# Optimization experiments

Measured on AMD Instinct MI355X. Metric: run time of the kernel, lower is better.

The kernel has to match this reference:

```python
import jax, jax.numpy as jnp
import numpy as np

B, S, HIDDEN = 2, 2048, 1024
HEADS, HEAD_DIM = 16, 64
GRID_SIZE, SPLINE_ORDER = 5, 3  # efficient-kan defaults


def b_splines(x, grid, k=SPLINE_ORDER):
    """x: (N, in), grid: (in, GRID_SIZE + 2k + 1) -> (N, in, GRID_SIZE + k)."""
    xe = x[..., None]
    bases = ((xe >= grid[:, :-1]) & (xe < grid[:, 1:])).astype(x.dtype)
    for p in range(1, k + 1):  # Cox-de Boor recursion, fixed small loop
        left = (xe - grid[:, : -(p + 1)]) / (grid[:, p:-1] - grid[:, : -(p + 1)]) * bases[..., :-1]
        right = (grid[:, p + 1:] - xe) / (grid[:, p + 1:] - grid[:, 1:-p]) * bases[..., 1:]
        bases = left + right
    return bases


def setup_inputs() -> dict:
    key = jax.random.key(0)
    ks = jax.random.split(key, 7)
    h = 2.0 / GRID_SIZE  # grid_range = [-1, 1]
    grid_1d = (jnp.arange(-SPLINE_ORDER, GRID_SIZE + SPLINE_ORDER + 1, dtype=jnp.float32) * h - 1.0)
    grid = jnp.tile(grid_1d[None, :], (HIDDEN, 1))  # (in, 12)
    return {
        "x": jax.random.normal(ks[0], (B, S, HIDDEN), jnp.float32),
        "base_weight": jax.random.normal(ks[1], (3 * HIDDEN, HIDDEN), jnp.float32) * 0.02,
        "spline_weight": jax.random.normal(ks[2], (3 * HIDDEN, HIDDEN, GRID_SIZE + SPLINE_ORDER), jnp.float32) * 0.02,
        "spline_scaler": jax.random.normal(ks[3], (3 * HIDDEN, HIDDEN), jnp.float32) * 0.1 + 1.0,
        "grid": grid,
        "rotation_matrix": jax.random.normal(ks[4], (HEAD_DIM, HEAD_DIM), jnp.float32) / np.sqrt(HEAD_DIM),
        "out_w": jax.random.normal(ks[5], (HIDDEN, HIDDEN), jnp.float32) * 0.02,
        "out_b": jnp.zeros((HIDDEN,), jnp.float32),
    }


def reference(x, base_weight, spline_weight, spline_scaler, grid, rotation_matrix, out_w, out_b):
    Bc, Sc, Hc = x.shape
    xf = x.reshape(-1, Hc)  # (N, in)
    # KANLinear: silu base branch + B-spline branch
    base = jax.nn.silu(xf) @ base_weight.T  # (N, 3H)
    bs = b_splines(xf, grid)  # (N, in, G+k)
    sw = spline_weight * spline_scaler[..., None]  # scaled spline weight
    spline = bs.reshape(bs.shape[0], -1) @ sw.reshape(sw.shape[0], -1).T
    qkv = (base + spline).reshape(Bc, Sc, HEADS, 3 * HEAD_DIM).transpose(0, 2, 1, 3)
    q, k, v = jnp.split(qkv, 3, axis=-1)  # each (B,H,S,dh)
    # RoPE via full learned rotation matrix
    qr = jnp.einsum('bhsd,md->bhsm', q, rotation_matrix)
    kr = jnp.einsum('bhsd,md->bhsm', k, rotation_matrix)
    scores = jnp.einsum('bhsm,bhtm->bhst', qr, kr) / (HEAD_DIM ** 0.5)
    attn = jax.nn.softmax(scores, axis=-1)
    ctx = jnp.einsum('bhst,bhtd->bhsd', attn, v)
    ctx = ctx.transpose(0, 2, 1, 3).reshape(Bc, Sc, Hc)
    return ctx @ out_w.T + out_b
```

## Files before the change

### kernel.cpp

```cpp
#include <hip/hip_runtime.h>
#include <cstdint>
#include <cstddef>

typedef __bf16 bf16;
typedef bf16  bf16x8 __attribute__((ext_vector_type(8)));
typedef float f32x4  __attribute__((ext_vector_type(4)));

#define GLOBAL_AS __attribute__((address_space(1)))
#define LDS_AS    __attribute__((address_space(3)))

__device__ __forceinline__ void ldg_lds16(const void* g, void* l) {
  __builtin_amdgcn_global_load_lds((const GLOBAL_AS void*)g, (LDS_AS void*)l, 16, 0, 0);
}

constexpr int NB    = 2;
constexpr int SQ    = 2048;
constexpr int HID   = 1024;
constexpr int NHEAD = 16;
constexpr int HD    = 64;
constexpr int NROW  = NB * SQ;
constexpr int KA    = HID + HID * 8;
constexpr int NO    = 3 * HID;

__global__ __launch_bounds__(256) void build_a(const float* __restrict__ X,
                                               const float* __restrict__ Grid,
                                               bf16* __restrict__ A) {
  int idx = blockIdx.x * 256 + threadIdx.x;
  int n = idx >> 10, i = idx & 1023;
  float x = X[idx];
  float s = x / (1.0f + __expf(-x));
  A[(size_t)n * KA + i] = (bf16)s;

  float kn[12];
#pragma unroll
  for (int t = 0; t < 12; t++) kn[t] = Grid[i * 12 + t];
  float bs[11];
#pragma unroll
  for (int t = 0; t < 11; t++) bs[t] = (x >= kn[t] && x < kn[t + 1]) ? 1.0f : 0.0f;
#pragma unroll
  for (int p = 1; p <= 3; p++) {
#pragma unroll
    for (int t = 0; t + p < 11; t++) {
      bs[t] = (x - kn[t]) / (kn[t + p] - kn[t]) * bs[t]
            + (kn[t + p + 1] - x) / (kn[t + p + 1] - kn[t + 1]) * bs[t + 1];
    }
  }
  union { bf16 h[8]; uint4 u; } pk;
#pragma unroll
  for (int t = 0; t < 8; t++) pk.h[t] = (bf16)bs[t];
  *(uint4*)(A + (size_t)n * KA + HID + i * 8) = pk.u;
}

__global__ __launch_bounds__(256) void build_w(const float* __restrict__ BW,
                                               const float* __restrict__ SW,
                                               const float* __restrict__ SS,
                                               bf16* __restrict__ Wp) {
  int idx = blockIdx.x * 256 + threadIdx.x;
  int o = idx / 1152;
  int jc = idx - o * 1152;
  float4 f0, f1;
  if (jc < 128) {
    f0 = *(const float4*)(BW + (size_t)o * HID + jc * 8);
    f1 = *(const float4*)(BW + (size_t)o * HID + jc * 8 + 4);
  } else {
    int ii = jc - 128;
    float sc = SS[(size_t)o * HID + ii];
    f0 = *(const float4*)(SW + ((size_t)o * HID + ii) * 8);
    f1 = *(const float4*)(SW + ((size_t)o * HID + ii) * 8 + 4);
    f0.x *= sc; f0.y *= sc; f0.z *= sc; f0.w *= sc;
    f1.x *= sc; f1.y *= sc; f1.z *= sc; f1.w *= sc;
  }
  union { bf16 h[8]; uint4 u; } pk;
  pk.h[0] = (bf16)f0.x; pk.h[1] = (bf16)f0.y; pk.h[2] = (bf16)f0.z; pk.h[3] = (bf16)f0.w;
  pk.h[4] = (bf16)f1.x; pk.h[5] = (bf16)f1.y; pk.h[6] = (bf16)f1.z; pk.h[7] = (bf16)f1.w;
  *(uint4*)(Wp + (size_t)o * KA + jc * 8) = pk.u;
}

__global__ __launch_bounds__(256) void conv_wout(const float* __restrict__ OW,
                                                 bf16* __restrict__ WOB) {
  int i = (blockIdx.x * 256 + threadIdx.x) * 4;
  float4 f = *(const float4*)(OW + i);
  union { bf16 h[4]; uint2 u; } p;
  p.h[0] = (bf16)f.x; p.h[1] = (bf16)f.y; p.h[2] = (bf16)f.z; p.h[3] = (bf16)f.w;
  *(uint2*)(WOB + i) = p.u;
}

__global__ __launch_bounds__(256) void compute_m(const float* __restrict__ R,
                                                 bf16* __restrict__ Mb) {
  __shared__ float Rl[64 * 64];
  int tid = threadIdx.x;
  for (int idx = tid; idx < 4096; idx += 256) Rl[idx] = R[idx];
  __syncthreads();
  int d = tid >> 2;
  int e0 = (tid & 3) * 16;
#pragma unroll
  for (int j = 0; j < 16; j++) {
    int e = e0 + j;
    float acc = 0.f;
#pragma unroll
    for (int m = 0; m < 64; m++) acc += Rl[m * 64 + d] * Rl[m * 64 + e];
    Mb[d * 64 + e] = (bf16)(0.125f * acc);
  }
}

template <int K>
__device__ __forceinline__ void gemm_tile(const bf16* __restrict__ A,
                                          const bf16* __restrict__ Bw,
                                          int rowBase, int colBase,
                                          bf16* As, bf16* Bs, f32x4 acc[4][4]) {
  const int tid  = threadIdx.x;
  const int lane = tid & 63, wave = tid >> 6;
  const int wm = (wave >> 1) * 64, wn = (wave & 1) * 64;
  const int l15 = lane & 15, quad = lane >> 4;
  const int rA = tid >> 2;
  const int swSrc = ((tid & 3) ^ ((rA >> 1) & 3)) * 8;
  const int swRd  = (quad ^ ((l15 >> 1) & 3)) * 8;
#pragma unroll
  for (int mi = 0; mi < 4; mi++)
#pragma unroll
    for (int ni = 0; ni < 4; ni++) acc[mi][ni] = (f32x4){0.f, 0.f, 0.f, 0.f};

  const bf16* Ag1 = A  + (size_t)(rowBase + rA) * K + swSrc;
  const bf16* Ag2 = A  + (size_t)(rowBase + 64 + rA) * K + swSrc;
  const bf16* Bg1 = Bw + (size_t)(colBase + rA) * K + swSrc;
  const bf16* Bg2 = Bw + (size_t)(colBase + 64 + rA) * K + swSrc;

  for (int k0 = 0; k0 < K; k0 += 32) {
    __syncthreads();
    ldg_lds16(Ag1 + k0, As + tid * 8);
    ldg_lds16(Ag2 + k0, As + 2048 + tid * 8);
    ldg_lds16(Bg1 + k0, Bs + tid * 8);
    ldg_lds16(Bg2 + k0, Bs + 2048 + tid * 8);
    __syncthreads();
    bf16x8 af[4], bfr[4];
#pragma unroll
    for (int mi = 0; mi < 4; mi++)
      af[mi] = *(const bf16x8*)(As + (wm + mi * 16 + l15) * 32 + swRd);
#pragma unroll
    for (int ni = 0; ni < 4; ni++)
      bfr[ni] = *(const bf16x8*)(Bs + (wn + ni * 16 + l15) * 32 + swRd);
#pragma unroll
    for (int mi = 0; mi < 4; mi++)
#pragma unroll
      for (int ni = 0; ni < 4; ni++)
        acc[mi][ni] = __builtin_amdgcn_mfma_f32_16x16x32_bf16(af[mi], bfr[ni], acc[mi][ni], 0, 0, 0);
  }
}

__global__ __launch_bounds__(256) void gemm_qkv(const bf16* __restrict__ A,
                                                const bf16* __restrict__ W,
                                                bf16* __restrict__ QQ,
                                                bf16* __restrict__ KK,
                                                bf16* __restrict__ VV) {
  __shared__ __align__(16) bf16 As[128 * 32];
  __shared__ __align__(16) bf16 Bs[128 * 32];
  f32x4 acc[4][4];
  const int rowBase = blockIdx.y * 128, colBase = blockIdx.x * 128;
  gemm_tile<KA>(A, W, rowBase, colBase, As, Bs, acc);

  const int tid = threadIdx.x, lane = tid & 63, wave = tid >> 6;
  const int wm = (wave >> 1) * 64, wn = (wave & 1) * 64;
  const int l15 = lane & 15, quad = lane >> 4;
#pragma unroll
  for (int mi = 0; mi < 4; mi++)
#pragma unroll
    for (int ni = 0; ni < 4; ni++)
#pragma unroll
      for (int r = 0; r < 4; r++) {
        int row = rowBase + wm + mi * 16 + quad * 4 + r;
        int col = colBase + wn + ni * 16 + l15;
        int b = row >> 11, s = row & 2047;
        int hh = col / 192, c = col - hh * 192;
        size_t base = ((size_t)(b * NHEAD + hh) * SQ + s) * HD;
        float v = acc[mi][ni][r];
        if (c < 64)        QQ[base + c] = (bf16)v;
        else if (c < 128)  KK[base + c - 64] = (bf16)v;
        else               VV[base + c - 128] = (bf16)v;
      }
}

__global__ __launch_bounds__(256) void transpose_v(const bf16* __restrict__ VV,
                                                   bf16* __restrict__ VT) {
  __shared__ __align__(16) bf16 Ts[64 * 72];
  const int st = blockIdx.x, bh = blockIdx.y, tid = threadIdx.x;
  const bf16* src = VV + ((size_t)bh * SQ + st * 64) * HD;
#pragma unroll
  for (int i = 0; i < 2; i++) {
    int c = i * 256 + tid, row = c >> 3, seg = c & 7;
    bf16x8 v8 = *(const bf16x8*)(src + row * HD + seg * 8);
    *(bf16x8*)(&Ts[row * 72 + seg * 8]) = v8;
  }
  __syncthreads();
#pragma unroll
  for (int i = 0; i < 2; i++) {
    int c = i * 256 + tid, drow = c >> 3, seg = c & 7;
    bf16x8 o8;
#pragma unroll
    for (int j = 0; j < 8; j++) o8[j] = Ts[(seg * 8 + j) * 72 + drow];
    *(bf16x8*)(VT + ((size_t)bh * HD + drow) * SQ + st * 64 + seg * 8) = o8;
  }
}

__global__ __launch_bounds__(256) void attn(const bf16* __restrict__ QQ,
                                            const bf16* __restrict__ KK,
                                            const bf16* __restrict__ VT,
                                            const bf16* __restrict__ Mb,
                                            bf16* __restrict__ CTXB) {
  __shared__ __align__(16) bf16 Qs[128 * 64];
  __shared__ __align__(16) bf16 Ks[128 * 64];
  __shared__ __align__(16) bf16 Vt[64 * 128];
  __shared__ __align__(16) bf16 Ps[128 * 64];
  __shared__ __align__(16) bf16 Ms[64 * 64];
  const int bh = blockIdx.y;
  const int b = bh >> 4, h = bh & 15;
  const int qbase = blockIdx.x * 128;
  const bf16* Q  = QQ + (size_t)bh * SQ * HD;
  const bf16* Kp = KK + (size_t)bh * SQ * HD;
  const bf16* Vp = VT + (size_t)bh * HD * SQ;
  const int tid = threadIdx.x, lane = tid & 63, wave = tid >> 6;
  const int l15 = lane & 15, quad = lane >> 4;
  const int sw8 = l15 & 7;
  const float SHIFT = 12.0f;

#pragma unroll
  for (int i = 0; i < 4; i++) {
    int c = i * 256 + tid, row = c >> 3, seg = c & 7;
    ldg_lds16(Q + (size_t)(qbase + row) * HD + ((seg ^ (row & 7)) * 8), Qs + c * 8);
  }
#pragma unroll
  for (int i = 0; i < 2; i++) {
    int c = i * 256 + tid, row = c >> 3, seg = c & 7;
    ldg_lds16(Mb + row * 64 + ((seg ^ (row & 7)) * 8), Ms + c * 8);
  }
  __syncthreads();

  {
    f32x4 racc[2][4];
#pragma unroll
    for (int mi = 0; mi < 2; mi++)
#pragma unroll
      for (int nj = 0; nj < 4; nj++) racc[mi][nj] = (f32x4){0.f, 0.f, 0.f, 0.f};
#pragma unroll
    for (int kc = 0; kc < 2; kc++) {
      const int slot = ((kc * 4 + quad) ^ sw8) * 8;
      bf16x8 aq[2], bm[4];
#pragma unroll
      for (int mi = 0; mi < 2; mi++)
        aq[mi] = *(const bf16x8*)(Qs + (wave * 32 + mi * 16 + l15) * 64 + slot);
#pragma unroll
      for (int nj = 0; nj < 4; nj++)
        bm[nj] = *(const bf16x8*)(Ms + (nj * 16 + l15) * 64 + slot);
#pragma unroll
      for (int mi = 0; mi < 2; mi++)
#pragma unroll
        for (int nj = 0; nj < 4; nj++)
          racc[mi][nj] = __builtin_amdgcn_mfma_f32_16x16x32_bf16(aq[mi], bm[nj], racc[mi][nj], 0, 0, 0);
    }
#pragma unroll
    for (int mi = 0; mi < 2; mi++)
#pragma unroll
      for (int nj = 0; nj < 4; nj++)
#pragma unroll
        for (int r = 0; r < 4; r++) {
          int qrow = wave * 32 + mi * 16 + quad * 4 + r;
          int slot = ((nj * 2 + (l15 >> 3)) ^ (qrow & 7)) * 8 + (l15 & 7);
          Qs[qrow * 64 + slot] = (bf16)racc[mi][nj][r];
        }
  }
  bf16x8 qf[2][2];
#pragma unroll
  for (int kc = 0; kc < 2; kc++)
#pragma unroll
    for (int mi = 0; mi < 2; mi++)
      qf[mi][kc] = *(const bf16x8*)(Qs + (wave * 32 + mi * 16 + l15) * 64 + (((kc * 4 + quad) ^ sw8) * 8));

  float lpart[2][4];
  f32x4 ctxacc[2][4];
#pragma unroll
  for (int mi = 0; mi < 2; mi++)
#pragma unroll
    for (int r = 0; r < 4; r++) lpart[mi][r] = 0.f;
#pragma unroll
  for (int mi = 0; mi < 2; mi++)
#pragma unroll
    for (int nd = 0; nd < 4; nd++) ctxacc[mi][nd] = (f32x4){0.f, 0.f, 0.f, 0.f};

  for (int kt = 0; kt < SQ / 128; kt++) {
    const int kbase = kt * 128;
    if (kt) __syncthreads();
#pragma unroll
    for (int i = 0; i < 4; i++) {
      int c = i * 256 + tid, row = c >> 3, seg = c & 7;
      ldg_lds16(Kp + (size_t)(kbase + row) * HD + ((seg ^ (row & 7)) * 8), Ks + c * 8);
    }
#pragma unroll
    for (int i = 0; i < 4; i++) {
      int c = i * 256 + tid, row = c >> 4, seg = c & 15;
      ldg_lds16(Vp + (size_t)row * SQ + kbase + ((seg ^ (row & 7)) * 8), Vt + c * 8);
    }
    __syncthreads();

#pragma unroll
    for (int hh = 0; hh < 2; hh++) {
      f32x4 sacc[2][4];
#pragma unroll
      for (int mi = 0; mi < 2; mi++)
#pragma unroll
        for (int nj = 0; nj < 4; nj++) sacc[mi][nj] = (f32x4){0.f, 0.f, 0.f, 0.f};
#pragma unroll
      for (int kc = 0; kc < 2; kc++) {
        const int slot = ((kc * 4 + quad) ^ sw8) * 8;
        bf16x8 bfr[4];
#pragma unroll
        for (int nj = 0; nj < 4; nj++)
          bfr[nj] = *(const bf16x8*)(Ks + (hh * 64 + nj * 16 + l15) * 64 + slot);
#pragma unroll
        for (int mi = 0; mi < 2; mi++)
#pragma unroll
          for (int nj = 0; nj < 4; nj++)
            sacc[mi][nj] = __builtin_amdgcn_mfma_f32_16x16x32_bf16(qf[mi][kc], bfr[nj], sacc[mi][nj], 0, 0, 0);
      }
#pragma unroll
      for (int mi = 0; mi < 2; mi++)
#pragma unroll
        for (int nj = 0; nj < 4; nj++)
#pragma unroll
          for (int r = 0; r < 4; r++) {
            float p = __expf(sacc[mi][nj][r] - SHIFT);
            lpart[mi][r] += p;
            int prow = wave * 32 + mi * 16 + quad * 4 + r;
            int slot = ((nj * 2 + (l15 >> 3)) ^ (prow & 7)) * 8 + (l15 & 7);
            Ps[prow * 64 + slot] = (bf16)p;
          }
#pragma unroll
      for (int kc = 0; kc < 2; kc++) {
        const int aslot = ((kc * 4 + quad) ^ sw8) * 8;
        const int vslot = (((hh * 8 + kc * 4 + quad)) ^ sw8) * 8;
        bf16x8 af[2], bfr[4];
#pragma unroll
        for (int mi = 0; mi < 2; mi++)
          af[mi] = *(const bf16x8*)(Ps + (wave * 32 + mi * 16 + l15) * 64 + aslot);
#pragma unroll
        for (int nd = 0; nd < 4; nd++)
          bfr[nd] = *(const bf16x8*)(Vt + (nd * 16 + l15) * 128 + vslot);
#pragma unroll
        for (int mi = 0; mi < 2; mi++)
#pragma unroll
          for (int nd = 0; nd < 4; nd++)
            ctxacc[mi][nd] = __builtin_amdgcn_mfma_f32_16x16x32_bf16(af[mi], bfr[nd], ctxacc[mi][nd], 0, 0, 0);
      }
    }
  }

#pragma unroll
  for (int mi = 0; mi < 2; mi++)
#pragma unroll
    for (int r = 0; r < 4; r++) {
      float l = lpart[mi][r];
#pragma unroll
      for (int off = 1; off < 16; off <<= 1) l += __shfl_xor(l, off);
      float inv = 1.0f / l;
#pragma unroll
      for (int nd = 0; nd < 4; nd++) {
        int srow = qbase + wave * 32 + mi * 16 + quad * 4 + r;
        float val = ctxacc[mi][nd][r] * inv;
        CTXB[(size_t)(b * SQ + srow) * HID + h * HD + nd * 16 + l15] = (bf16)val;
      }
    }
}

__global__ __launch_bounds__(256) void gemm_out(const bf16* __restrict__ CTX,
                                                const bf16* __restrict__ WOB,
                                                const float* __restrict__ OB,
                                                float* __restrict__ OUT) {
  __shared__ __align__(16) bf16 As[128 * 32];
  __shared__ __align__(16) bf16 Bs[128 * 32];
  f32x4 acc[4][4];
  const int rowBase = blockIdx.y * 128, colBase = blockIdx.x * 128;
  gemm_tile<HID>(CTX, WOB, rowBase, colBase, As, Bs, acc);

  const int tid = threadIdx.x, lane = tid & 63, wave = tid >> 6;
  const int wm = (wave >> 1) * 64, wn = (wave & 1) * 64;
  const int l15 = lane & 15, quad = lane >> 4;
#pragma unroll
  for (int mi = 0; mi < 4; mi++)
#pragma unroll
    for (int ni = 0; ni < 4; ni++)
#pragma unroll
      for (int r = 0; r < 4; r++) {
        int row = rowBase + wm + mi * 16 + quad * 4 + r;
        int col = colBase + wn + ni * 16 + l15;
        OUT[(size_t)row * HID + col] = acc[mi][ni][r] + OB[col];
      }
}

extern "C" void kernel_launch(void* const* d_in, const int* in_sizes, int n_in,
                              void* d_out, int out_size, void* d_ws, size_t ws_size,
                              hipStream_t stream) {
  const float* x    = (const float*)d_in[0];
  const float* bw   = (const float*)d_in[1];
  const float* sw   = (const float*)d_in[2];
  const float* ss   = (const float*)d_in[3];
  const float* grid = (const float*)d_in[4];
  const float* rot  = (const float*)d_in[5];
  const float* ow   = (const float*)d_in[6];
  const float* ob   = (const float*)d_in[7];
  float* out = (float*)d_out;

  char* ws = (char*)d_ws;
  bf16* Aact = (bf16*)(ws);
  bf16* vt   = (bf16*)(ws);
  bf16* Mb   = (bf16*)(ws + 8388608);
  bf16* Wp   = (bf16*)(ws + 75497472);
  bf16* qq   = (bf16*)(ws + 132120576);
  bf16* kk   = (bf16*)(ws + 140509184);
  bf16* vv   = (bf16*)(ws + 148897792);
  bf16* ctxb = (bf16*)(ws + 157286400);
  bf16* wob  = (bf16*)(ws + 165675008);

  build_a<<<NROW * HID / 256, 256, 0, stream>>>(x, grid, Aact);
  build_w<<<NO * (KA / 8) / 256, 256, 0, stream>>>(bw, sw, ss, Wp);
  conv_wout<<<HID * HID / 1024, 256, 0, stream>>>(ow, wob);
  gemm_qkv<<<dim3(NO / 128, NROW / 128), 256, 0, stream>>>(Aact, Wp, qq, kk, vv);
  compute_m<<<1, 256, 0, stream>>>(rot, Mb);
  transpose_v<<<dim3(SQ / 64, NB * NHEAD), 256, 0, stream>>>(vv, vt);
  attn<<<dim3(SQ / 128, NB * NHEAD), 256, 0, stream>>>(qq, kk, vt, Mb, ctxb);
  gemm_out<<<dim3(HID / 128, NROW / 128), 256, 0, stream>>>(ctxb, wob, ob, out);
}
```

Before: 631.2 us.

## Rewrite QKV GEMM with 256x192 tiles, double-buffered BK=64 LDS pipeline

Replaces the 128x128, BK=32 single-buffered QKV GEMM with a 512-thread kernel using 256x192 tiles (one head per column block), BK=64, XOR-swizzled LDS, and double-buffered async global-to-LDS loads overlapped with MFMA. Aligning the column tile to one head simplifies the scatter epilogue, and the larger tile raises operand reuse. The cost is heavier register and LDS use (about 112KB LDS per block) and a smaller grid of 256 blocks, which may hurt occupancy and load balance.

```diff
diff --git a/kernel.cpp b/kernel.cpp
--- a/kernel.cpp
+++ b/kernel.cpp
@@ -147,32 +147,116 @@
   }
 }
 
-__global__ __launch_bounds__(256) void gemm_qkv(const bf16* __restrict__ A,
-                                                const bf16* __restrict__ W,
-                                                bf16* __restrict__ QQ,
-                                                bf16* __restrict__ KK,
-                                                bf16* __restrict__ VV) {
-  __shared__ __align__(16) bf16 As[128 * 32];
-  __shared__ __align__(16) bf16 Bs[128 * 32];
-  f32x4 acc[4][4];
-  const int rowBase = blockIdx.y * 128, colBase = blockIdx.x * 128;
-  gemm_tile<KA>(A, W, rowBase, colBase, As, Bs, acc);
-
-  const int tid = threadIdx.x, lane = tid & 63, wave = tid >> 6;
-  const int wm = (wave >> 1) * 64, wn = (wave & 1) * 64;
+__global__ __launch_bounds__(512, 2) void gemm_qkv(const bf16* __restrict__ A,
+                                                   const bf16* __restrict__ W,
+                                                   bf16* __restrict__ QQ,
+                                                   bf16* __restrict__ KK,
+                                                   bf16* __restrict__ VV) {
+  constexpr int BM = 256, BN = 192, BK = 64;
+  constexpr int NT = KA / BK;
+  __shared__ __align__(16) bf16 As[2 * BM * BK];
+  __shared__ __align__(16) bf16 Bs[2 * BN * BK];
+  const int tid  = threadIdx.x;
+  const int lane = tid & 63, wave = tid >> 6;
+  const int wr = wave >> 2, wc = wave & 3;
   const int l15 = lane & 15, quad = lane >> 4;
-#pragma unroll
-  for (int mi = 0; mi < 4; mi++)
-#pragma unroll
-    for (int ni = 0; ni < 4; ni++)
+  const int xw = l15 & 7;
+  const int rowBase = blockIdx.y * BM;
+  const int colBase = blockIdx.x * BN;
+
+  int aRow[4], aOff[4];
+#pragma unroll
+  for (int i = 0; i < 4; i++) {
+    int c = i * 512 + tid;
+    aRow[i] = c >> 3;
+    aOff[i] = ((c & 7) ^ (aRow[i] & 7)) * 8;
+  }
+  int bRow[3], bOff[3];
+#pragma unroll
+  for (int i = 0; i < 3; i++) {
+    int c = i * 512 + tid;
+    bRow[i] = c >> 3;
+    bOff[i] = ((c & 7) ^ (bRow[i] & 7)) * 8;
+  }
+  const int dstBase = tid * 8;
+
+  auto stage = [&](int t, int b) {
+    const bf16* Asrc = A + (size_t)rowBase * KA + (size_t)t * BK;
+    const bf16* Bsrc = W + (size_t)colBase * KA + (size_t)t * BK;
+    bf16* Ad = As + b * (BM * BK);
+    bf16* Bd = Bs + b * (BN * BK);
+#pragma unroll
+    for (int i = 0; i < 4; i++)
+      ldg_lds16(Asrc + (size_t)aRow[i] * KA + aOff[i], Ad + i * 4096 + dstBase);
+#pragma unroll
+    for (int i = 0; i < 3; i++)
+      ldg_lds16(Bsrc + (size_t)bRow[i] * KA + bOff[i], Bd + i * 4096 + dstBase);
+  };
+
+  f32x4 acc[8][3];
+#pragma unroll
+  for (int mi = 0; mi < 8; mi++)
+#pragma unroll
+    for (int nj = 0; nj < 3; nj++) acc[mi][nj] = (f32x4){0.f, 0.f, 0.f, 0.f};
+
+  stage(0, 0);
+  stage(1, 1);
+  asm volatile("s_waitcnt vmcnt(7)\n\ts_barrier" ::: "memory");
+
+  auto tile_step = [&](int t, int b) {
+    const bf16* Ab = As + b * (BM * BK);
+    const bf16* Bb = Bs + b * (BN * BK);
+    bf16x8 af[2][8], bfv[2][3];
+#pragma unroll
+    for (int kc = 0; kc < 2; kc++) {
+      const int slot = ((kc * 4 + quad) ^ xw) * 8;
+#pragma unroll
+      for (int mi = 0; mi < 8; mi++)
+        af[kc][mi] = *(const bf16x8*)(Ab + (wr * 128 + mi * 16 + l15) * 64 + slot);
+#pragma unroll
+      for (int nj = 0; nj < 3; nj++)
+        bfv[kc][nj] = *(const bf16x8*)(Bb + (wc * 48 + nj * 16 + l15) * 64 + slot);
+    }
+    __builtin_amdgcn_s_setprio(1);
+#pragma unroll
+    for (int mi = 0; mi < 8; mi++)
+#pragma unroll
+      for (int nj = 0; nj < 3; nj++)
+        acc[mi][nj] = __builtin_amdgcn_mfma_f32_16x16x32_bf16(af[0][mi], bfv[0][nj], acc[mi][nj], 0, 0, 0);
+    __builtin_amdgcn_s_setprio(0);
+    asm volatile("s_waitcnt lgkmcnt(0)\n\ts_barrier" ::: "memory");
+    if (t + 2 < NT) stage(t + 2, b);
+    __builtin_amdgcn_s_setprio(1);
+#pragma unroll
+    for (int mi = 0; mi < 8; mi++)
+#pragma unroll
+      for (int nj = 0; nj < 3; nj++)
+        acc[mi][nj] = __builtin_amdgcn_mfma_f32_16x16x32_bf16(af[1][mi], bfv[1][nj], acc[mi][nj], 0, 0, 0);
+    __builtin_amdgcn_s_setprio(0);
+    if (t + 2 < NT)
+      asm volatile("s_waitcnt vmcnt(7)\n\ts_barrier" ::: "memory");
+    else
+      asm volatile("s_waitcnt vmcnt(0)\n\ts_barrier" ::: "memory");
+  };
+
+#pragma unroll 1
+  for (int t = 0; t < NT; t += 2) {
+    tile_step(t, 0);
+    tile_step(t + 1, 1);
+  }
+
+  const int h = blockIdx.x;
+#pragma unroll
+  for (int mi = 0; mi < 8; mi++)
+#pragma unroll
+    for (int nj = 0; nj < 3; nj++)
 #pragma unroll
       for (int r = 0; r < 4; r++) {
-        int row = rowBase + wm + mi * 16 + quad * 4 + r;
-        int col = colBase + wn + ni * 16 + l15;
+        int row = rowBase + wr * 128 + mi * 16 + quad * 4 + r;
+        int c = wc * 48 + nj * 16 + l15;
         int b = row >> 11, s = row & 2047;
-        int hh = col / 192, c = col - hh * 192;
-        size_t base = ((size_t)(b * NHEAD + hh) * SQ + s) * HD;
-        float v = acc[mi][ni][r];
+        size_t base = ((size_t)(b * NHEAD + h) * SQ + s) * HD;
+        float v = acc[mi][nj][r];
         if (c < 64)        QQ[base + c] = (bf16)v;
         else if (c < 128)  KK[base + c - 64] = (bf16)v;
         else               VV[base + c - 128] = (bf16)v;
@@ -421,7 +505,7 @@
   build_a<<<NROW * HID / 256, 256, 0, stream>>>(x, grid, Aact);
   build_w<<<NO * (KA / 8) / 256, 256, 0, stream>>>(bw, sw, ss, Wp);
   conv_wout<<<HID * HID / 1024, 256, 0, stream>>>(ow, wob);
-  gemm_qkv<<<dim3(NO / 128, NROW / 128), 256, 0, stream>>>(Aact, Wp, qq, kk, vv);
+  gemm_qkv<<<dim3(NO / 192, NROW / 256), 512, 0, stream>>>(Aact, Wp, qq, kk, vv);
   compute_m<<<1, 256, 0, stream>>>(rot, Mb);
   transpose_v<<<dim3(SQ / 64, NB * NHEAD), 256, 0, stream>>>(vv, vt);
   attn<<<dim3(SQ / 128, NB * NHEAD), 256, 0, stream>>>(qq, kk, vt, Mb, ctxb);
```

Measured after the change: 645.1 us. +2.2%, slower.

## Rewrite QKV GEMM with 256x256 tiles, double-buffered LDS and XCD-aware block remap

Applied to the files above, without the earlier changes.

Replaces the QKV GEMM's 128x128 single-buffered tile with a 256x256 tile computed by 8 waves. It uses double-buffered LDS with async global-to-LDS loads interleaved between MFMA phases, plus s_setprio around the MFMA bursts. Block IDs are remapped so neighbouring tiles land on the same XCD for better L2 reuse. This targets the dominant K=9216 GEMM's memory stalls and load/compute serialization. In exchange it uses more registers and LDS (128KB per block) and relies on hand-placed barriers and waitcnts.

```diff
diff --git a/kernel.cpp b/kernel.cpp
--- a/kernel.cpp
+++ b/kernel.cpp
@@ -147,32 +147,122 @@
   }
 }
 
-__global__ __launch_bounds__(256) void gemm_qkv(const bf16* __restrict__ A,
-                                                const bf16* __restrict__ W,
-                                                bf16* __restrict__ QQ,
-                                                bf16* __restrict__ KK,
-                                                bf16* __restrict__ VV) {
-  __shared__ __align__(16) bf16 As[128 * 32];
-  __shared__ __align__(16) bf16 Bs[128 * 32];
-  f32x4 acc[4][4];
-  const int rowBase = blockIdx.y * 128, colBase = blockIdx.x * 128;
-  gemm_tile<KA>(A, W, rowBase, colBase, As, Bs, acc);
-
-  const int tid = threadIdx.x, lane = tid & 63, wave = tid >> 6;
-  const int wm = (wave >> 1) * 64, wn = (wave & 1) * 64;
+#define QKV_STAGE(gbase, growBase, ldsBase, t_, kc_, bufSel)                      \
+  {                                                                               \
+    const size_t ko_ = (size_t)(t_) * 64 + (kc_) * 32;                            \
+    bf16* dp_ = (ldsBase) + ((bufSel) * 2 + (kc_)) * 8192;                        \
+    ldg_lds16((gbase) + (size_t)((growBase) + rS0) * KA + ko_ + kOff0, dp_ + tid * 8); \
+    ldg_lds16((gbase) + (size_t)((growBase) + rS1) * KA + ko_ + kOff1, dp_ + 4096 + tid * 8); \
+  }
+
+#define QKV_RDA(dst, H, kc_, bufSel)                                              \
+  _Pragma("unroll") for (int i_ = 0; i_ < 4; i_++)                                \
+      dst[i_] = *(const bf16x8*)(As + ((bufSel) * 2 + (kc_)) * 8192 +             \
+                                 (wr * 128 + (H) * 64 + i_ * 16 + l15) * 32 + sw16);
+
+#define QKV_RDB(dst, kc_, bufSel)                                                 \
+  _Pragma("unroll") for (int j_ = 0; j_ < 4; j_++)                                \
+      dst[j_] = *(const bf16x8*)(Bs + ((bufSel) * 2 + (kc_)) * 8192 +             \
+                                 (wc * 64 + j_ * 16 + l15) * 32 + sw16);
+
+#define QKV_MM16(H)                                                               \
+  {                                                                               \
+    __builtin_amdgcn_s_setprio(1);                                                \
+    _Pragma("unroll") for (int i_ = 0; i_ < 4; i_++)                              \
+        _Pragma("unroll") for (int j_ = 0; j_ < 4; j_++)                          \
+            acc[(H) * 4 + i_][j_] = __builtin_amdgcn_mfma_f32_16x16x32_bf16(      \
+                a[i_], b[j_], acc[(H) * 4 + i_][j_], 0, 0, 0);                    \
+    __builtin_amdgcn_s_setprio(0);                                                \
+  }
+
+__global__ __launch_bounds__(512, 2) void gemm_qkv(const bf16* __restrict__ A,
+                                                   const bf16* __restrict__ W,
+                                                   bf16* __restrict__ QQ,
+                                                   bf16* __restrict__ KK,
+                                                   bf16* __restrict__ VV) {
+  constexpr int NT = KA / 64;
+  __shared__ __align__(16) bf16 As[2 * 2 * 256 * 32];
+  __shared__ __align__(16) bf16 Bs[2 * 2 * 256 * 32];
+  const int tid  = threadIdx.x;
+  const int lane = tid & 63, wave = tid >> 6;
+  const int wr = wave >> 2, wc = wave & 3;
   const int l15 = lane & 15, quad = lane >> 4;
-#pragma unroll
-  for (int mi = 0; mi < 4; mi++)
-#pragma unroll
-    for (int ni = 0; ni < 4; ni++)
+  const int sw16 = (quad ^ ((l15 >> 1) & 3)) * 8;
+
+  const int hwid  = blockIdx.y * 12 + blockIdx.x;
+  const int newid = (hwid & 7) * 24 + (hwid >> 3);
+  const int rowBase = (newid & 15) * 256;
+  const int colBase = (newid >> 4) * 256;
+
+  const int rS0 = tid >> 2, rS1 = 128 + (tid >> 2);
+  const int sl = tid & 3;
+  const int kOff0 = (sl ^ ((rS0 >> 1) & 3)) * 8;
+  const int kOff1 = (sl ^ ((rS1 >> 1) & 3)) * 8;
+
+  f32x4 acc[8][4];
+#pragma unroll
+  for (int mi = 0; mi < 8; mi++)
+#pragma unroll
+    for (int nj = 0; nj < 4; nj++) acc[mi][nj] = (f32x4){0.f, 0.f, 0.f, 0.f};
+
+  QKV_STAGE(A, rowBase, As, 0, 0, 0);
+  QKV_STAGE(W, colBase, Bs, 0, 0, 0);
+  QKV_STAGE(A, rowBase, As, 0, 1, 0);
+  QKV_STAGE(W, colBase, Bs, 0, 1, 0);
+  asm volatile("s_waitcnt vmcnt(4)\n\ts_barrier" ::: "memory");
+
+#pragma unroll 1
+  for (int t = 0; t < NT; t++) {
+    const int buf = t & 1, nbuf = buf ^ 1;
+    bf16x8 a[4], b[4];
+    QKV_RDA(a, 0, 0, buf);
+    QKV_RDB(b, 0, buf);
+    if (t + 1 < NT) QKV_STAGE(A, rowBase, As, t + 1, 0, nbuf);
+    __builtin_amdgcn_s_barrier();
+    asm volatile("s_waitcnt lgkmcnt(0)" ::: "memory");
+    QKV_MM16(0);
+    __builtin_amdgcn_s_barrier();
+    QKV_RDA(a, 1, 0, buf);
+    if (t + 1 < NT) QKV_STAGE(W, colBase, Bs, t + 1, 0, nbuf);
+    __builtin_amdgcn_s_barrier();
+    asm volatile("s_waitcnt lgkmcnt(0)" ::: "memory");
+    QKV_MM16(1);
+    if (t + 1 < NT) {
+      asm volatile("s_waitcnt vmcnt(4)\n\ts_barrier" ::: "memory");
+    } else {
+      asm volatile("s_waitcnt vmcnt(0)\n\ts_barrier" ::: "memory");
+    }
+    QKV_RDA(a, 0, 1, buf);
+    QKV_RDB(b, 1, buf);
+    if (t + 1 < NT) QKV_STAGE(A, rowBase, As, t + 1, 1, nbuf);
+    __builtin_amdgcn_s_barrier();
+    asm volatile("s_waitcnt lgkmcnt(0)" ::: "memory");
+    QKV_MM16(0);
+    __builtin_amdgcn_s_barrier();
+    QKV_RDA(a, 1, 1, buf);
+    if (t + 1 < NT) QKV_STAGE(W, colBase, Bs, t + 1, 1, nbuf);
+    __builtin_amdgcn_s_barrier();
+    asm volatile("s_waitcnt lgkmcnt(0)" ::: "memory");
+    QKV_MM16(1);
+    if (t + 1 < NT) {
+      asm volatile("s_waitcnt vmcnt(4)\n\ts_barrier" ::: "memory");
+    } else {
+      asm volatile("s_waitcnt vmcnt(0)\n\ts_barrier" ::: "memory");
+    }
+  }
+
+#pragma unroll
+  for (int mi = 0; mi < 8; mi++)
+#pragma unroll
+    for (int nj = 0; nj < 4; nj++)
 #pragma unroll
       for (int r = 0; r < 4; r++) {
-        int row = rowBase + wm + mi * 16 + quad * 4 + r;
-        int col = colBase + wn + ni * 16 + l15;
-        int b = row >> 11, s = row & 2047;
-        int hh = col / 192, c = col - hh * 192;
-        size_t base = ((size_t)(b * NHEAD + hh) * SQ + s) * HD;
-        float v = acc[mi][ni][r];
+        int row = rowBase + wr * 128 + mi * 16 + quad * 4 + r;
+        int col = colBase + wc * 64 + nj * 16 + l15;
+        int bb = row >> 11, s = row & 2047;
+        int h = col / 192, c = col - h * 192;
+        size_t base = ((size_t)(bb * NHEAD + h) * SQ + s) * HD;
+        float v = acc[mi][nj][r];
         if (c < 64)        QQ[base + c] = (bf16)v;
         else if (c < 128)  KK[base + c - 64] = (bf16)v;
         else               VV[base + c - 128] = (bf16)v;
@@ -421,7 +511,7 @@
   build_a<<<NROW * HID / 256, 256, 0, stream>>>(x, grid, Aact);
   build_w<<<NO * (KA / 8) / 256, 256, 0, stream>>>(bw, sw, ss, Wp);
   conv_wout<<<HID * HID / 1024, 256, 0, stream>>>(ow, wob);
-  gemm_qkv<<<dim3(NO / 128, NROW / 128), 256, 0, stream>>>(Aact, Wp, qq, kk, vv);
+  gemm_qkv<<<dim3(12, 16), 512, 0, stream>>>(Aact, Wp, qq, kk, vv);
   compute_m<<<1, 256, 0, stream>>>(rot, Mb);
   transpose_v<<<dim3(SQ / 64, NB * NHEAD), 256, 0, stream>>>(vv, vt);
   attn<<<dim3(SQ / 128, NB * NHEAD), 256, 0, stream>>>(qq, kk, vt, Mb, ctxb);
```

Measured after the change: 677.2 us. +7.3%, slower.
